# Performance work log

Hardware: AMD Instinct MI355X
Metric: run time of the kernel (lower is better)

## Reference

```python
import jax, jax.numpy as jnp
import numpy as np

N = 50000      # nodes
E = 800000     # directed edges (before self-loops)
IN = 128       # input feature dim
HID = 32       # per-head hidden channels
HEADS = 4
OUT = 16       # output classes
NEG_SLOPE = 0.2


def setup_inputs() -> dict:
    key = jax.random.key(0)
    ks = jax.random.split(key, 14)
    x = jax.random.normal(ks[0], (N, IN), jnp.float32)
    edge_index = jax.random.randint(ks[1], (2, E), 0, N, dtype=jnp.int64)

    def glorot(k, shape):
        fan = shape[0] + shape[-1]
        s = np.sqrt(6.0 / fan).astype(np.float32)
        return jax.random.uniform(k, shape, jnp.float32, -s, s)

    return {
        "x": x,
        "edge_index": edge_index,
        # layer 0: IN -> HEADS*HID
        "W1": glorot(ks[2], (IN, HEADS * HID)),
        "a_src1": glorot(ks[3], (HEADS, HID)),
        "a_dst1": glorot(ks[4], (HEADS, HID)),
        "b1": jnp.zeros((HEADS * HID,), jnp.float32),
        # layer 1: HEADS*HID -> HEADS*HID
        "W2": glorot(ks[5], (HEADS * HID, HEADS * HID)),
        "a_src2": glorot(ks[6], (HEADS, HID)),
        "a_dst2": glorot(ks[7], (HEADS, HID)),
        "b2": jnp.zeros((HEADS * HID,), jnp.float32),
        # layer 2: HEADS*HID -> OUT, heads=1
        "W3": glorot(ks[8], (HEADS * HID, OUT)),
        "a_src3": glorot(ks[9], (1, OUT)),
        "a_dst3": glorot(ks[10], (1, OUT)),
        "b3": jnp.zeros((OUT,), jnp.float32),
    }


def _gat_layer(x, src, dst, W, a_s, a_d, b):
    """One PyG-style GATConv (eval mode). src/dst include self-loops."""
    H, C = a_s.shape
    h = (x @ W).reshape(N, H, C)                       # [N,H,C]
    e_src = jnp.einsum('nhc,hc->nh', h, a_s)           # [N,H]
    e_dst = jnp.einsum('nhc,hc->nh', h, a_d)
    e = jax.nn.leaky_relu(e_src[src] + e_dst[dst], NEG_SLOPE)   # [E',H]
    # segment softmax over incoming edges of each target node
    m = jax.ops.segment_max(e, dst, num_segments=N)    # [N,H]
    p = jnp.exp(e - m[dst])
    denom = jax.ops.segment_sum(p, dst, num_segments=N)
    alpha = p / (denom[dst] + 1e-16)                   # [E',H]
    out = jax.ops.segment_sum(alpha[:, :, None] * h[src], dst, num_segments=N)
    return out.reshape(N, H * C) + b


def reference(x, edge_index, W1, a_src1, a_dst1, b1, W2, a_src2, a_dst2, b2,
              W3, a_src3, a_dst3, b3):
    loops = jnp.arange(N, dtype=edge_index.dtype)
    src = jnp.concatenate([edge_index[0], loops])
    dst = jnp.concatenate([edge_index[1], loops])
    h = jax.nn.relu(_gat_layer(x, src, dst, W1, a_src1, a_dst1, b1))
    h = jax.nn.relu(_gat_layer(h, src, dst, W2, a_src2, a_dst2, b2))
    return _gat_layer(h, src, dst, W3, a_src3, a_dst3, b3)   # [N, OUT]
```

## Files before the change

### kernel.cpp

```cpp
#include <hip/hip_runtime.h>

#define NODES 50000
#define EDGES 800000
#define EPLUS (EDGES + NODES)
#define GEMMBLK 782
#define FILLBLK 3328
#define CHUNKE 2048
#define NRANGE 8
#define RSPAN 6250
#define CAP 64

typedef __attribute__((ext_vector_type(8))) short bf16x8;
typedef __attribute__((ext_vector_type(4))) float f32x4;
typedef __attribute__((ext_vector_type(4))) short short4v;

__device__ __forceinline__ float ld_f(const void* p, int isbf, size_t i) {
    if (isbf) return __uint_as_float(((unsigned)((const unsigned short*)p)[i]) << 16);
    return ((const float*)p)[i];
}
__device__ __forceinline__ int ld_idx(const int* ei, int i64, int elem) {
    int v = i64 ? ei[(size_t)elem * 2] : ei[elem];
    v = v < 0 ? 0 : v;
    return v >= NODES ? NODES - 1 : v;
}
__device__ __forceinline__ unsigned short f2bf(float f) {
    unsigned u = __float_as_uint(f);
    u = u + 0x7FFFu + ((u >> 16) & 1u);
    return (unsigned short)(u >> 16);
}
__device__ __forceinline__ unsigned pack2bf(float a, float b) {
    return (unsigned)f2bf(a) | ((unsigned)f2bf(b) << 16);
}
__device__ __forceinline__ float bflo(unsigned u) { return __uint_as_float(u << 16); }
__device__ __forceinline__ float bfhi(unsigned u) { return __uint_as_float(u & 0xFFFF0000u); }

__device__ __forceinline__ void detect_flags(const unsigned* xw, const int* eiw,
                                             int* sh, int& isbf, int& i64) {
    const int t = threadIdx.x;
    if (t < 2) sh[t] = 0;
    __syncthreads();
    if (t < 256) {
        unsigned lo = xw[t] & 0xFFFFu;
        int e = (int)((lo >> 7) & 0xFF);
        if (lo == 0u || (e >= 90 && e <= 140)) atomicAdd(&sh[0], 1);
    }
    if (t < 64) {
        if (eiw[2 * t + 1] == 0) atomicAdd(&sh[1], 1);
    }
    __syncthreads();
    isbf = sh[0] > 200 ? 1 : 0;
    i64  = sh[1] > 48 ? 1 : 0;
}

#define O_W1 0
#define O_AS1 16384
#define O_AD1 16512
#define O_B1 16640
#define O_W2 16768
#define O_AS2 33152
#define O_AD2 33280
#define O_B2 33408
#define O_W3 33536
#define O_AS3 35584
#define O_AD3 35600
#define O_B3 35616
#define W_TOTAL 35632

#define PB_CNT 196
#define PB_WC 140
#define PB_F1 64
#define PB_F2 64
#define PB_F3 8
#define PREP_GRID (PB_CNT + PB_WC + PB_F1 + PB_F2 + PB_F3)

__global__ __launch_bounds__(256) void k_prep(
        const unsigned* __restrict__ xraw, const int* __restrict__ ei,
        const void* w1, const void* as1, const void* ad1, const void* b1,
        const void* w2, const void* as2, const void* ad2, const void* b2,
        const void* w3, const void* as3, const void* ad3, const void* b3,
        float* __restrict__ Wc, int* __restrict__ cnt,
        unsigned short* __restrict__ W1fh, unsigned short* __restrict__ W1fl,
        unsigned short* __restrict__ W2fh, unsigned short* __restrict__ W2fl,
        unsigned short* __restrict__ W3fh, unsigned short* __restrict__ W3fl) {
    __shared__ int sh[2];
    const int t = threadIdx.x;
    int isbf, i64;
    detect_flags(xraw, ei, sh, isbf, i64);
    (void)i64;

    int b = blockIdx.x;
    if (b < PB_CNT) {
        int i = b * 256 + t;
        if (i < NODES) cnt[i] = 0;
        return;
    }
    b -= PB_CNT;
    if (b < PB_WC) {
        const int f = b * 256 + t;
        if (f < W_TOTAL) {
            const int sz[12] = {16384,128,128,128,16384,128,128,128,2048,16,16,16};
            const void* ps[12] = {w1,as1,ad1,b1,w2,as2,ad2,b2,w3,as3,ad3,b3};
            int off = 0;
#pragma unroll
            for (int s = 0; s < 12; ++s) {
                if (f >= off && f < off + sz[s]) Wc[f] = ld_f(ps[s], isbf, f - off);
                off += sz[s];
            }
        }
        return;
    }
    b -= PB_WC;
    const void* wsrc; unsigned short *fh, *fl; int ncols; int e;
    if (b < PB_F1)                { wsrc = w1; fh = W1fh; fl = W1fl; ncols = 128; e = b * 256 + t; }
    else if (b < PB_F1 + PB_F2)   { wsrc = w2; fh = W2fh; fl = W2fl; ncols = 128; e = (b - PB_F1) * 256 + t; }
    else                          { wsrc = w3; fh = W3fh; fl = W3fl; ncols = 16;  e = (b - PB_F1 - PB_F2) * 256 + t; }
    const int j = e & 7, l = (e >> 3) & 63;
    int nf, kc;
    if (ncols == 128) { nf = (e >> 9) & 7; kc = e >> 12; }
    else              { nf = 0;            kc = (e >> 9) & 3; }
    const int k = kc * 32 + (l >> 4) * 4 + (j & 3) + (j >> 2) * 16;
    const int n = nf * 16 + (l & 15);
    const float v = ld_f(wsrc, isbf, (size_t)k * ncols + n);
    const unsigned short hi = f2bf(v);
    const float res = v - __uint_as_float(((unsigned)hi) << 16);
    fh[e] = hi;
    fl[e] = f2bf(res);
}

__global__ __launch_bounds__(256, 4) void k_fillgemm1(
        const unsigned* __restrict__ xraw, const int* __restrict__ ei,
        const unsigned short* __restrict__ W1fh, const unsigned short* __restrict__ W1fl,
        const float* __restrict__ Wc,
        unsigned short* __restrict__ hout, float* __restrict__ es, float* __restrict__ ed,
        int* __restrict__ cnt, unsigned short* __restrict__ col) {
    __shared__ int sh[2];
    const int t = threadIdx.x;
    int isbf, i64;
    detect_flags(xraw, ei, sh, isbf, i64);

    if (blockIdx.x >= GEMMBLK) {
        const int fb = blockIdx.x - GEMMBLK;
        const int r  = blockIdx.x & 7;
        const int chunk = fb >> 3;
        const int lo = r * RSPAN, hi = lo + RSPAN;
        const int base = chunk * CHUNKE;
#pragma unroll
        for (int it = 0; it < CHUNKE / 256; ++it) {
            const int e = base + it * 256 + t;
            if (e >= EPLUS) continue;
            int s, d;
            if (e < EDGES) {
                d = ld_idx(ei, i64, EDGES + e);
                if (d < lo || d >= hi) continue;
                s = ld_idx(ei, i64, e);
            } else {
                s = d = e - EDGES;
                if (d < lo || d >= hi) continue;
            }
            int slot = atomicAdd(&cnt[d], 1);
            if (slot < CAP) col[d * CAP + slot] = (unsigned short)s;
        }
        return;
    }

    __shared__ unsigned short Ah[4 * 64 * 8];
    __shared__ unsigned short Al[4 * 64 * 8];
    const int rowBase = blockIdx.x * 64;
    const int w = t >> 6, lane = t & 63;

    f32x4 acc[4][2];
#pragma unroll
    for (int mf = 0; mf < 4; ++mf)
#pragma unroll
        for (int nn = 0; nn < 2; ++nn) acc[mf][nn] = (f32x4){0.f, 0.f, 0.f, 0.f};

    for (int kc = 0; kc < 4; ++kc) {
        __syncthreads();
#pragma unroll
        for (int u = 0; u < 2; ++u) {
            const int f = t + 256 * u;
            const int r = f >> 3, c4 = f & 7;
            int gr = rowBase + r; if (gr >= NODES) gr = NODES - 1;
            const int mf = r >> 4;
            const int l  = (r & 15) + 16 * (c4 & 3);
            const int j0 = 4 * (c4 >> 2);
            const int di = (mf * 64 + l) * 8 + j0;
            if (!isbf) {
                f32x4 v = __builtin_nontemporal_load(
                    (const f32x4*)((const float*)xraw + (size_t)gr * 128 + kc * 32 + c4 * 4));
                const unsigned short h0 = f2bf(v[0]), h1 = f2bf(v[1]), h2 = f2bf(v[2]), h3 = f2bf(v[3]);
                short4v hv = {(short)h0, (short)h1, (short)h2, (short)h3};
                *(short4v*)&Ah[di] = hv;
                short4v lv = {(short)f2bf(v[0] - __uint_as_float((unsigned)h0 << 16)),
                              (short)f2bf(v[1] - __uint_as_float((unsigned)h1 << 16)),
                              (short)f2bf(v[2] - __uint_as_float((unsigned)h2 << 16)),
                              (short)f2bf(v[3] - __uint_as_float((unsigned)h3 << 16))};
                *(short4v*)&Al[di] = lv;
            } else {
                short4v v = __builtin_nontemporal_load(
                    (const short4v*)((const unsigned short*)xraw + (size_t)gr * 128 + kc * 32 + c4 * 4));
                *(short4v*)&Ah[di] = v;
            }
        }
        __syncthreads();
        const int nA = 2 * w, nB = 2 * w + 1;
        const bf16x8 bh0 = *(const bf16x8*)(W1fh + (((size_t)kc * 8 + nA) * 64 + lane) * 8);
        const bf16x8 bh1 = *(const bf16x8*)(W1fh + (((size_t)kc * 8 + nB) * 64 + lane) * 8);
        const bf16x8 bl0 = *(const bf16x8*)(W1fl + (((size_t)kc * 8 + nA) * 64 + lane) * 8);
        const bf16x8 bl1 = *(const bf16x8*)(W1fl + (((size_t)kc * 8 + nB) * 64 + lane) * 8);
#pragma unroll
        for (int mf = 0; mf < 4; ++mf) {
            const bf16x8 ah = *(const bf16x8*)&Ah[(mf * 64 + lane) * 8];
            acc[mf][0] = __builtin_amdgcn_mfma_f32_16x16x32_bf16(ah, bh0, acc[mf][0], 0, 0, 0);
            acc[mf][1] = __builtin_amdgcn_mfma_f32_16x16x32_bf16(ah, bh1, acc[mf][1], 0, 0, 0);
            if (!isbf) {
                const bf16x8 al = *(const bf16x8*)&Al[(mf * 64 + lane) * 8];
                acc[mf][0] = __builtin_amdgcn_mfma_f32_16x16x32_bf16(ah, bl0, acc[mf][0], 0, 0, 0);
                acc[mf][1] = __builtin_amdgcn_mfma_f32_16x16x32_bf16(ah, bl1, acc[mf][1], 0, 0, 0);
                acc[mf][0] = __builtin_amdgcn_mfma_f32_16x16x32_bf16(al, bh0, acc[mf][0], 0, 0, 0);
                acc[mf][1] = __builtin_amdgcn_mfma_f32_16x16x32_bf16(al, bh1, acc[mf][1], 0, 0, 0);
            }
        }
    }

    const int colA = 32 * w + (lane & 15), colB = colA + 16;
    const float asA = Wc[O_AS1 + colA], asB = Wc[O_AS1 + colB];
    const float adA = Wc[O_AD1 + colA], adB = Wc[O_AD1 + colB];
    const int g = lane >> 4;
#pragma unroll
    for (int mf = 0; mf < 4; ++mf) {
#pragma unroll
        for (int r = 0; r < 4; ++r) {
            const int row = rowBase + mf * 16 + 4 * g + r;
            const bool ok = row < NODES;
            const float vA = acc[mf][0][r], vB = acc[mf][1][r];
            if (ok) {
                hout[(size_t)row * 128 + colA] = f2bf(vA);
                hout[(size_t)row * 128 + colB] = f2bf(vB);
            }
            float se = vA * asA + vB * asB;
            float sd = vA * adA + vB * adB;
#pragma unroll
            for (int off = 1; off < 16; off <<= 1) {
                se += __shfl_xor(se, off);
                sd += __shfl_xor(sd, off);
            }
            if (ok && (lane & 15) == 0) {
                es[row * 4 + w] = se;
                ed[row * 4 + w] = sd;
            }
        }
    }
}

__device__ __forceinline__ void gather4_node(
        int nd, const int* __restrict__ cnt, const unsigned short* __restrict__ col,
        const float* __restrict__ esi, const float* __restrict__ edi,
        const uint4* __restrict__ h4, int esub, int c, int myh,
        float a[8], float& den) {
    int deg = cnt[nd]; deg = deg < CAP ? deg : CAP;
    const int start = nd * CAP;
    const float edh = edi[nd * 4 + myh];
#pragma unroll
    for (int j = 0; j < 8; ++j) a[j] = 0.f;
    den = 0.f;
    int e = esub;
    for (; e + 12 < deg; e += 16) {
        int s0 = col[start + e];
        int s1 = col[start + e + 4];
        int s2 = col[start + e + 8];
        int s3 = col[start + e + 12];
        uint4 u0 = h4[(size_t)s0 * 16 + c];
        uint4 u1 = h4[(size_t)s1 * 16 + c];
        uint4 u2 = h4[(size_t)s2 * 16 + c];
        uint4 u3 = h4[(size_t)s3 * 16 + c];
        float v0 = esi[s0 * 4 + myh] + edh; v0 = v0 > 0.f ? v0 : 0.2f * v0;
        float v1 = esi[s1 * 4 + myh] + edh; v1 = v1 > 0.f ? v1 : 0.2f * v1;
        float v2 = esi[s2 * 4 + myh] + edh; v2 = v2 > 0.f ? v2 : 0.2f * v2;
        float v3 = esi[s3 * 4 + myh] + edh; v3 = v3 > 0.f ? v3 : 0.2f * v3;
        float p0 = __expf(v0), p1 = __expf(v1), p2 = __expf(v2), p3 = __expf(v3);
        den += (p0 + p1) + (p2 + p3);
        a[0] += p0 * bflo(u0.x) + p1 * bflo(u1.x) + p2 * bflo(u2.x) + p3 * bflo(u3.x);
        a[1] += p0 * bfhi(u0.x) + p1 * bfhi(u1.x) + p2 * bfhi(u2.x) + p3 * bfhi(u3.x);
        a[2] += p0 * bflo(u0.y) + p1 * bflo(u1.y) + p2 * bflo(u2.y) + p3 * bflo(u3.y);
        a[3] += p0 * bfhi(u0.y) + p1 * bfhi(u1.y) + p2 * bfhi(u2.y) + p3 * bfhi(u3.y);
        a[4] += p0 * bflo(u0.z) + p1 * bflo(u1.z) + p2 * bflo(u2.z) + p3 * bflo(u3.z);
        a[5] += p0 * bfhi(u0.z) + p1 * bfhi(u1.z) + p2 * bfhi(u2.z) + p3 * bfhi(u3.z);
        a[6] += p0 * bflo(u0.w) + p1 * bflo(u1.w) + p2 * bflo(u2.w) + p3 * bflo(u3.w);
        a[7] += p0 * bfhi(u0.w) + p1 * bfhi(u1.w) + p2 * bfhi(u2.w) + p3 * bfhi(u3.w);
    }
    for (; e + 4 < deg; e += 8) {
        int s0 = col[start + e];
        int s1 = col[start + e + 4];
        uint4 u0 = h4[(size_t)s0 * 16 + c];
        uint4 u1 = h4[(size_t)s1 * 16 + c];
        float v0 = esi[s0 * 4 + myh] + edh; v0 = v0 > 0.f ? v0 : 0.2f * v0;
        float v1 = esi[s1 * 4 + myh] + edh; v1 = v1 > 0.f ? v1 : 0.2f * v1;
        float p0 = __expf(v0);
        float p1 = __expf(v1);
        den += p0 + p1;
        a[0] += p0 * bflo(u0.x) + p1 * bflo(u1.x);
        a[1] += p0 * bfhi(u0.x) + p1 * bfhi(u1.x);
        a[2] += p0 * bflo(u0.y) + p1 * bflo(u1.y);
        a[3] += p0 * bfhi(u0.y) + p1 * bfhi(u1.y);
        a[4] += p0 * bflo(u0.z) + p1 * bflo(u1.z);
        a[5] += p0 * bfhi(u0.z) + p1 * bfhi(u1.z);
        a[6] += p0 * bflo(u0.w) + p1 * bflo(u1.w);
        a[7] += p0 * bfhi(u0.w) + p1 * bfhi(u1.w);
    }
    for (; e < deg; e += 4) {
        int s0 = col[start + e];
        uint4 u0 = h4[(size_t)s0 * 16 + c];
        float v0 = esi[s0 * 4 + myh] + edh; v0 = v0 > 0.f ? v0 : 0.2f * v0;
        float p0 = __expf(v0);
        den += p0;
        a[0] += p0 * bflo(u0.x);
        a[1] += p0 * bfhi(u0.x);
        a[2] += p0 * bflo(u0.y);
        a[3] += p0 * bfhi(u0.y);
        a[4] += p0 * bflo(u0.z);
        a[5] += p0 * bfhi(u0.z);
        a[6] += p0 * bflo(u0.w);
        a[7] += p0 * bfhi(u0.w);
    }
    den += __shfl_xor(den, 16);
    den += __shfl_xor(den, 32);
#pragma unroll
    for (int j = 0; j < 8; ++j) {
        a[j] += __shfl_xor(a[j], 16);
        a[j] += __shfl_xor(a[j], 32);
    }
}

__global__ __launch_bounds__(512, 4) void k_gg128(
        const int* __restrict__ cnt, const unsigned short* __restrict__ col,
        const float* __restrict__ esi, const float* __restrict__ edi,
        const unsigned short* __restrict__ hfeat, const float* __restrict__ bias,
        const unsigned short* __restrict__ Wfh, const unsigned short* __restrict__ Wfl,
        const float* __restrict__ a_s, const float* __restrict__ a_d,
        unsigned short* __restrict__ hout, float* __restrict__ eso, float* __restrict__ edo) {
    __shared__ unsigned short X2f[4 * 4 * 64 * 8];
    const int t = threadIdx.x;
    const int v = t >> 6, lane = t & 63;
    const int rowBase = blockIdx.x * 64;

    const int esub = lane >> 4;
    const int c = lane & 15;
    const int myh = c >> 2;
    const uint4* __restrict__ h4 = (const uint4*)hfeat;
    for (int i = 0; i < 8; ++i) {
        const int r = v * 8 + i;
        const int nd = rowBase + r;
        if (nd >= NODES) break;
        float a[8], den;
        gather4_node(nd, cnt, col, esi, edi, h4, esub, c, myh, a, den);
        if (esub == 0) {
            const float inv = 1.f / (den + 1e-16f);
            float4 b0 = ((const float4*)bias)[c * 2];
            float4 b1 = ((const float4*)bias)[c * 2 + 1];
            float o0 = a[0]*inv + b0.x, o1 = a[1]*inv + b0.y;
            float o2 = a[2]*inv + b0.z, o3 = a[3]*inv + b0.w;
            float o4 = a[4]*inv + b1.x, o5 = a[5]*inv + b1.y;
            float o6 = a[6]*inv + b1.z, o7 = a[7]*inv + b1.w;
            o0 = o0 > 0.f ? o0 : 0.f;  o1 = o1 > 0.f ? o1 : 0.f;
            o2 = o2 > 0.f ? o2 : 0.f;  o3 = o3 > 0.f ? o3 : 0.f;
            o4 = o4 > 0.f ? o4 : 0.f;  o5 = o5 > 0.f ? o5 : 0.f;
            o6 = o6 > 0.f ? o6 : 0.f;  o7 = o7 > 0.f ? o7 : 0.f;
            const int cc = c & 3;
            const int kc = c >> 2;
            const int mf = r >> 4;
            const int l0 = (r & 15) + 16 * ((2 * cc) & 3);
            const int l1 = (r & 15) + 16 * ((2 * cc + 1) & 3);
            const int j0 = (cc < 2) ? 0 : 4;
            short4v w0 = {(short)f2bf(o0), (short)f2bf(o1), (short)f2bf(o2), (short)f2bf(o3)};
            short4v w1 = {(short)f2bf(o4), (short)f2bf(o5), (short)f2bf(o6), (short)f2bf(o7)};
            *(short4v*)&X2f[((kc * 4 + mf) * 64 + l0) * 8 + j0] = w0;
            *(short4v*)&X2f[((kc * 4 + mf) * 64 + l1) * 8 + j0] = w1;
        }
    }
    __syncthreads();

    const int vr = v >> 2, vc = v & 3;
    f32x4 acc[2][2];
#pragma unroll
    for (int m = 0; m < 2; ++m)
#pragma unroll
        for (int nn = 0; nn < 2; ++nn) acc[m][nn] = (f32x4){0.f, 0.f, 0.f, 0.f};

    const int nA = 2 * vc, nB = 2 * vc + 1;
#pragma unroll
    for (int kc = 0; kc < 4; ++kc) {
        const bf16x8 bh0 = *(const bf16x8*)(Wfh + (((size_t)kc * 8 + nA) * 64 + lane) * 8);
        const bf16x8 bh1 = *(const bf16x8*)(Wfh + (((size_t)kc * 8 + nB) * 64 + lane) * 8);
        const bf16x8 bl0 = *(const bf16x8*)(Wfl + (((size_t)kc * 8 + nA) * 64 + lane) * 8);
        const bf16x8 bl1 = *(const bf16x8*)(Wfl + (((size_t)kc * 8 + nB) * 64 + lane) * 8);
#pragma unroll
        for (int m = 0; m < 2; ++m) {
            const int mf = 2 * vr + m;
            const bf16x8 ah = *(const bf16x8*)&X2f[((kc * 4 + mf) * 64 + lane) * 8];
            acc[m][0] = __builtin_amdgcn_mfma_f32_16x16x32_bf16(ah, bh0, acc[m][0], 0, 0, 0);
            acc[m][1] = __builtin_amdgcn_mfma_f32_16x16x32_bf16(ah, bh1, acc[m][1], 0, 0, 0);
            acc[m][0] = __builtin_amdgcn_mfma_f32_16x16x32_bf16(ah, bl0, acc[m][0], 0, 0, 0);
            acc[m][1] = __builtin_amdgcn_mfma_f32_16x16x32_bf16(ah, bl1, acc[m][1], 0, 0, 0);
        }
    }

    const int colA = 32 * vc + (lane & 15), colB = colA + 16;
    const float asA = a_s[colA], asB = a_s[colB];
    const float adA = a_d[colA], adB = a_d[colB];
    const int g = lane >> 4;
#pragma unroll
    for (int m = 0; m < 2; ++m) {
#pragma unroll
        for (int r = 0; r < 4; ++r) {
            const int row = rowBase + (2 * vr + m) * 16 + 4 * g + r;
            const bool ok = row < NODES;
            const float vA = acc[m][0][r], vB = acc[m][1][r];
            if (ok) {
                hout[(size_t)row * 128 + colA] = f2bf(vA);
                hout[(size_t)row * 128 + colB] = f2bf(vB);
            }
            float se = vA * asA + vB * asB;
            float sd = vA * adA + vB * adB;
#pragma unroll
            for (int off = 1; off < 16; off <<= 1) {
                se += __shfl_xor(se, off);
                sd += __shfl_xor(sd, off);
            }
            if (ok && (lane & 15) == 0) {
                eso[row * 4 + vc] = se;
                edo[row * 4 + vc] = sd;
            }
        }
    }
}

__global__ __launch_bounds__(512, 4) void k_gg16(
        const int* __restrict__ cnt, const unsigned short* __restrict__ col,
        const float* __restrict__ esi, const float* __restrict__ edi,
        const unsigned short* __restrict__ hfeat, const float* __restrict__ bias,
        const unsigned short* __restrict__ Wfh, const unsigned short* __restrict__ Wfl,
        const float* __restrict__ a_s, const float* __restrict__ a_d,
        unsigned short* __restrict__ hout, float* __restrict__ eso, float* __restrict__ edo) {
    __shared__ unsigned short X2f[4 * 4 * 64 * 8];
    const int t = threadIdx.x;
    const int v = t >> 6, lane = t & 63;
    const int rowBase = blockIdx.x * 64;

    const int esub = lane >> 4;
    const int c = lane & 15;
    const int myh = c >> 2;
    const uint4* __restrict__ h4 = (const uint4*)hfeat;
    for (int i = 0; i < 8; ++i) {
        const int r = v * 8 + i;
        const int nd = rowBase + r;
        if (nd >= NODES) break;
        float a[8], den;
        gather4_node(nd, cnt, col, esi, edi, h4, esub, c, myh, a, den);
        if (esub == 0) {
            const float inv = 1.f / (den + 1e-16f);
            float4 b0 = ((const float4*)bias)[c * 2];
            float4 b1 = ((const float4*)bias)[c * 2 + 1];
            float o0 = a[0]*inv + b0.x, o1 = a[1]*inv + b0.y;
            float o2 = a[2]*inv + b0.z, o3 = a[3]*inv + b0.w;
            float o4 = a[4]*inv + b1.x, o5 = a[5]*inv + b1.y;
            float o6 = a[6]*inv + b1.z, o7 = a[7]*inv + b1.w;
            o0 = o0 > 0.f ? o0 : 0.f;  o1 = o1 > 0.f ? o1 : 0.f;
            o2 = o2 > 0.f ? o2 : 0.f;  o3 = o3 > 0.f ? o3 : 0.f;
            o4 = o4 > 0.f ? o4 : 0.f;  o5 = o5 > 0.f ? o5 : 0.f;
            o6 = o6 > 0.f ? o6 : 0.f;  o7 = o7 > 0.f ? o7 : 0.f;
            const int cc = c & 3;
            const int kc = c >> 2;
            const int mf = r >> 4;
            const int l0 = (r & 15) + 16 * ((2 * cc) & 3);
            const int l1 = (r & 15) + 16 * ((2 * cc + 1) & 3);
            const int j0 = (cc < 2) ? 0 : 4;
            short4v w0 = {(short)f2bf(o0), (short)f2bf(o1), (short)f2bf(o2), (short)f2bf(o3)};
            short4v w1 = {(short)f2bf(o4), (short)f2bf(o5), (short)f2bf(o6), (short)f2bf(o7)};
            *(short4v*)&X2f[((kc * 4 + mf) * 64 + l0) * 8 + j0] = w0;
            *(short4v*)&X2f[((kc * 4 + mf) * 64 + l1) * 8 + j0] = w1;
        }
    }
    __syncthreads();

    if (v < 4) {
        f32x4 acc = (f32x4){0.f, 0.f, 0.f, 0.f};
#pragma unroll
        for (int kc = 0; kc < 4; ++kc) {
            const bf16x8 bh = *(const bf16x8*)(Wfh + ((size_t)kc * 64 + lane) * 8);
            const bf16x8 bl = *(const bf16x8*)(Wfl + ((size_t)kc * 64 + lane) * 8);
            const bf16x8 ah = *(const bf16x8*)&X2f[((kc * 4 + v) * 64 + lane) * 8];
            acc = __builtin_amdgcn_mfma_f32_16x16x32_bf16(ah, bh, acc, 0, 0, 0);
            acc = __builtin_amdgcn_mfma_f32_16x16x32_bf16(ah, bl, acc, 0, 0, 0);
        }
        const int cc = lane & 15, g = lane >> 4;
        const float asv = a_s[cc], adv = a_d[cc];
#pragma unroll
        for (int r = 0; r < 4; ++r) {
            const int row = rowBase + v * 16 + 4 * g + r;
            const bool ok = row < NODES;
            if (ok) hout[(size_t)row * 16 + cc] = f2bf(acc[r]);
            float se = acc[r] * asv;
            float sd = acc[r] * adv;
#pragma unroll
            for (int off = 1; off < 16; off <<= 1) {
                se += __shfl_xor(se, off);
                sd += __shfl_xor(sd, off);
            }
            if (ok && cc == 0) { eso[row] = se; edo[row] = sd; }
        }
    }
}

__global__ void k_gather1(const int* __restrict__ cnt, const unsigned short* __restrict__ col,
                          const float* __restrict__ es, const float* __restrict__ ed,
                          const unsigned short* __restrict__ hfeat,
                          const float* __restrict__ bias, float* __restrict__ outf) {
    const int nd = blockIdx.x * 4 + (threadIdx.x >> 6);
    if (nd >= NODES) return;
    const int lane = threadIdx.x & 63;
    int deg = cnt[nd]; deg = deg < CAP ? deg : CAP;
    const int start = nd * CAP;

    const float edv = ed[nd];
    const int esub = lane >> 3;
    const int c = lane & 7;
    const unsigned* __restrict__ h1 = (const unsigned*)hfeat;
    float a0 = 0.f, a1 = 0.f, den = 0.f;

    int e = esub;
    for (; e + 24 < deg; e += 32) {
        int s0 = col[start + e];
        int s1 = col[start + e + 8];
        int s2 = col[start + e + 16];
        int s3 = col[start + e + 24];
        unsigned u0 = h1[(size_t)s0 * 8 + c];
        unsigned u1 = h1[(size_t)s1 * 8 + c];
        unsigned u2 = h1[(size_t)s2 * 8 + c];
        unsigned u3 = h1[(size_t)s3 * 8 + c];
        float v0 = es[s0] + edv; v0 = v0 > 0.f ? v0 : 0.2f * v0;
        float v1 = es[s1] + edv; v1 = v1 > 0.f ? v1 : 0.2f * v1;
        float v2 = es[s2] + edv; v2 = v2 > 0.f ? v2 : 0.2f * v2;
        float v3 = es[s3] + edv; v3 = v3 > 0.f ? v3 : 0.2f * v3;
        float p0 = __expf(v0), p1 = __expf(v1), p2 = __expf(v2), p3 = __expf(v3);
        den += (p0 + p1) + (p2 + p3);
        a0 += p0 * bflo(u0) + p1 * bflo(u1) + p2 * bflo(u2) + p3 * bflo(u3);
        a1 += p0 * bfhi(u0) + p1 * bfhi(u1) + p2 * bfhi(u2) + p3 * bfhi(u3);
    }
    for (; e + 8 < deg; e += 16) {
        int s0 = col[start + e];
        int s1 = col[start + e + 8];
        unsigned u0 = h1[(size_t)s0 * 8 + c];
        unsigned u1 = h1[(size_t)s1 * 8 + c];
        float v0 = es[s0] + edv; v0 = v0 > 0.f ? v0 : 0.2f * v0;
        float v1 = es[s1] + edv; v1 = v1 > 0.f ? v1 : 0.2f * v1;
        float p0 = __expf(v0);
        float p1 = __expf(v1);
        den += p0 + p1;
        a0 += p0 * bflo(u0) + p1 * bflo(u1);
        a1 += p0 * bfhi(u0) + p1 * bfhi(u1);
    }
    for (; e < deg; e += 8) {
        int s0 = col[start + e];
        unsigned u0 = h1[(size_t)s0 * 8 + c];
        float v0 = es[s0] + edv; v0 = v0 > 0.f ? v0 : 0.2f * v0;
        float p0 = __expf(v0);
        den += p0;
        a0 += p0 * bflo(u0);
        a1 += p0 * bfhi(u0);
    }
    den += __shfl_xor(den, 8);  a0 += __shfl_xor(a0, 8);  a1 += __shfl_xor(a1, 8);
    den += __shfl_xor(den, 16); a0 += __shfl_xor(a0, 16); a1 += __shfl_xor(a1, 16);
    den += __shfl_xor(den, 32); a0 += __shfl_xor(a0, 32); a1 += __shfl_xor(a1, 32);
    if (lane < 8) {
        const float inv = 1.f / (den + 1e-16f);
        float2 b = ((const float2*)bias)[c];
        ((float2*)outf)[(size_t)nd * 8 + c] = make_float2(a0 * inv + b.x, a1 * inv + b.y);
    }
}

extern "C" void kernel_launch(void* const* d_in, const int* in_sizes, int n_in,
                              void* d_out, int out_size, void* d_ws, size_t ws_size,
                              hipStream_t stream) {
    const int* ei = (const int*)d_in[1];
    const unsigned* xraw = (const unsigned*)d_in[0];
    float* out = (float*)d_out;

    char* p = (char*)d_ws;
    unsigned short* h2  = (unsigned short*)p; p += (size_t)NODES * 128 * 2;
    unsigned short* h1  = (unsigned short*)p; p += (size_t)NODES * 128 * 2;
    float*          es1 = (float*)p;          p += (size_t)NODES * 4 * 4;
    float*          ed1 = (float*)p;          p += (size_t)NODES * 4 * 4;
    float*          Wc  = (float*)p;          p += (size_t)W_TOTAL * 4;
    int*            cnt = (int*)p;            p += (size_t)NODES * 4;
    unsigned short* col = (unsigned short*)p; p += (size_t)NODES * CAP * 2;
    unsigned short* W1fh = (unsigned short*)p; p += 16384 * 2;
    unsigned short* W1fl = (unsigned short*)p; p += 16384 * 2;
    unsigned short* W2fh = (unsigned short*)p; p += 16384 * 2;
    unsigned short* W2fl = (unsigned short*)p; p += 16384 * 2;
    unsigned short* W3fh = (unsigned short*)p; p += 2048 * 2;
    unsigned short* W3fl = (unsigned short*)p; p += 2048 * 2;
    float*          es2 = (float*)p;          p += (size_t)NODES * 4 * 4;
    float*          ed2 = (float*)p;          p += (size_t)NODES * 4 * 4;

    k_prep<<<PREP_GRID, 256, 0, stream>>>(
        xraw, ei,
        d_in[2], d_in[3], d_in[4], d_in[5],
        d_in[6], d_in[7], d_in[8], d_in[9],
        d_in[10], d_in[11], d_in[12], d_in[13],
        Wc, cnt, W1fh, W1fl, W2fh, W2fl, W3fh, W3fl);

    k_fillgemm1<<<GEMMBLK + FILLBLK, 256, 0, stream>>>(
        xraw, ei, W1fh, W1fl, Wc, h1, es1, ed1, cnt, col);

    k_gg128<<<GEMMBLK, 512, 0, stream>>>(cnt, col, es1, ed1, h1, Wc + O_B1,
                                         W2fh, W2fl, Wc + O_AS2, Wc + O_AD2,
                                         h2, es2, ed2);
    k_gg16<<<GEMMBLK, 512, 0, stream>>>(cnt, col, es2, ed2, h2, Wc + O_B2,
                                        W3fh, W3fl, Wc + O_AS3, Wc + O_AD3,
                                        h1, es1, ed1);
    const int ggrid = (NODES + 3) / 4;
    k_gather1<<<ggrid, 256, 0, stream>>>(cnt, col, es1, ed1, h1, Wc + O_B3, out);
}
```

Baseline: 283.6 us.

## Halve gather-GEMM block size to 32 rows and drop 4-way unrolled gather loops

The fused gather+GEMM kernels for layers 2 and 3 now use 256-thread blocks covering 32 nodes instead of 512 threads covering 64. The grid doubles, and the MFMA work is remapped so each of the 4 waves handles two column fragments across both row fragments. The 4-way unrolled edge loops in the gather helpers are removed, which lowers register pressure and code size, leaving 2-way unrolled and scalar tails. The aim is better occupancy and load balance for an irregular, latency-bound gather. The cost is less memory-level parallelism per thread, and the weight fragments are reloaded by twice as many blocks.

```diff
diff --git a/kernel.cpp b/kernel.cpp
--- a/kernel.cpp
+++ b/kernel.cpp
@@ -4,6 +4,7 @@
 #define EDGES 800000
 #define EPLUS (EDGES + NODES)
 #define GEMMBLK 782
+#define GGBLK 1563
 #define FILLBLK 3328
 #define CHUNKE 2048
 #define NRANGE 8
@@ -27,9 +28,6 @@
     unsigned u = __float_as_uint(f);
     u = u + 0x7FFFu + ((u >> 16) & 1u);
     return (unsigned short)(u >> 16);
-}
-__device__ __forceinline__ unsigned pack2bf(float a, float b) {
-    return (unsigned)f2bf(a) | ((unsigned)f2bf(b) << 16);
 }
 __device__ __forceinline__ float bflo(unsigned u) { return __uint_as_float(u << 16); }
 __device__ __forceinline__ float bfhi(unsigned u) { return __uint_as_float(u & 0xFFFF0000u); }
@@ -265,30 +263,6 @@
     for (int j = 0; j < 8; ++j) a[j] = 0.f;
     den = 0.f;
     int e = esub;
-    for (; e + 12 < deg; e += 16) {
-        int s0 = col[start + e];
-        int s1 = col[start + e + 4];
-        int s2 = col[start + e + 8];
-        int s3 = col[start + e + 12];
-        uint4 u0 = h4[(size_t)s0 * 16 + c];
-        uint4 u1 = h4[(size_t)s1 * 16 + c];
-        uint4 u2 = h4[(size_t)s2 * 16 + c];
-        uint4 u3 = h4[(size_t)s3 * 16 + c];
-        float v0 = esi[s0 * 4 + myh] + edh; v0 = v0 > 0.f ? v0 : 0.2f * v0;
-        float v1 = esi[s1 * 4 + myh] + edh; v1 = v1 > 0.f ? v1 : 0.2f * v1;
-        float v2 = esi[s2 * 4 + myh] + edh; v2 = v2 > 0.f ? v2 : 0.2f * v2;
-        float v3 = esi[s3 * 4 + myh] + edh; v3 = v3 > 0.f ? v3 : 0.2f * v3;
-        float p0 = __expf(v0), p1 = __expf(v1), p2 = __expf(v2), p3 = __expf(v3);
-        den += (p0 + p1) + (p2 + p3);
-        a[0] += p0 * bflo(u0.x) + p1 * bflo(u1.x) + p2 * bflo(u2.x) + p3 * bflo(u3.x);
-        a[1] += p0 * bfhi(u0.x) + p1 * bfhi(u1.x) + p2 * bfhi(u2.x) + p3 * bfhi(u3.x);
-        a[2] += p0 * bflo(u0.y) + p1 * bflo(u1.y) + p2 * bflo(u2.y) + p3 * bflo(u3.y);
-        a[3] += p0 * bfhi(u0.y) + p1 * bfhi(u1.y) + p2 * bfhi(u2.y) + p3 * bfhi(u3.y);
-        a[4] += p0 * bflo(u0.z) + p1 * bflo(u1.z) + p2 * bflo(u2.z) + p3 * bflo(u3.z);
-        a[5] += p0 * bfhi(u0.z) + p1 * bfhi(u1.z) + p2 * bfhi(u2.z) + p3 * bfhi(u3.z);
-        a[6] += p0 * bflo(u0.w) + p1 * bflo(u1.w) + p2 * bflo(u2.w) + p3 * bflo(u3.w);
-        a[7] += p0 * bfhi(u0.w) + p1 * bfhi(u1.w) + p2 * bfhi(u2.w) + p3 * bfhi(u3.w);
-    }
     for (; e + 4 < deg; e += 8) {
         int s0 = col[start + e];
         int s1 = col[start + e + 4];
@@ -332,17 +306,44 @@
     }
 }
 
-__global__ __launch_bounds__(512, 4) void k_gg128(
+#define NMF 2
+__device__ __forceinline__ void place_frag(
+        unsigned short* __restrict__ X2f, int r, int c,
+        const float a[8], float den, const float* __restrict__ bias) {
+    const float inv = 1.f / (den + 1e-16f);
+    float4 b0 = ((const float4*)bias)[c * 2];
+    float4 b1 = ((const float4*)bias)[c * 2 + 1];
+    float o0 = a[0]*inv + b0.x, o1 = a[1]*inv + b0.y;
+    float o2 = a[2]*inv + b0.z, o3 = a[3]*inv + b0.w;
+    float o4 = a[4]*inv + b1.x, o5 = a[5]*inv + b1.y;
+    float o6 = a[6]*inv + b1.z, o7 = a[7]*inv + b1.w;
+    o0 = o0 > 0.f ? o0 : 0.f;  o1 = o1 > 0.f ? o1 : 0.f;
+    o2 = o2 > 0.f ? o2 : 0.f;  o3 = o3 > 0.f ? o3 : 0.f;
+    o4 = o4 > 0.f ? o4 : 0.f;  o5 = o5 > 0.f ? o5 : 0.f;
+    o6 = o6 > 0.f ? o6 : 0.f;  o7 = o7 > 0.f ? o7 : 0.f;
+    const int cc = c & 3;
+    const int kc = c >> 2;
+    const int mf = r >> 4;
+    const int l0 = (r & 15) + 16 * ((2 * cc) & 3);
+    const int l1 = (r & 15) + 16 * ((2 * cc + 1) & 3);
+    const int j0 = (cc < 2) ? 0 : 4;
+    short4v w0 = {(short)f2bf(o0), (short)f2bf(o1), (short)f2bf(o2), (short)f2bf(o3)};
+    short4v w1 = {(short)f2bf(o4), (short)f2bf(o5), (short)f2bf(o6), (short)f2bf(o7)};
+    *(short4v*)&X2f[((kc * NMF + mf) * 64 + l0) * 8 + j0] = w0;
+    *(short4v*)&X2f[((kc * NMF + mf) * 64 + l1) * 8 + j0] = w1;
+}
+
+__global__ __launch_bounds__(256, 8) void k_gg128(
         const int* __restrict__ cnt, const unsigned short* __restrict__ col,
         const float* __restrict__ esi, const float* __restrict__ edi,
         const unsigned short* __restrict__ hfeat, const float* __restrict__ bias,
         const unsigned short* __restrict__ Wfh, const unsigned short* __restrict__ Wfl,
         const float* __restrict__ a_s, const float* __restrict__ a_d,
         unsigned short* __restrict__ hout, float* __restrict__ eso, float* __restrict__ edo) {
-    __shared__ unsigned short X2f[4 * 4 * 64 * 8];
+    __shared__ unsigned short X2f[4 * NMF * 64 * 8];
     const int t = threadIdx.x;
     const int v = t >> 6, lane = t & 63;
-    const int rowBase = blockIdx.x * 64;
+    const int rowBase = blockIdx.x * 32;
 
     const int esub = lane >> 4;
     const int c = lane & 15;
@@ -354,40 +355,17 @@
         if (nd >= NODES) break;
         float a[8], den;
         gather4_node(nd, cnt, col, esi, edi, h4, esub, c, myh, a, den);
-        if (esub == 0) {
-            const float inv = 1.f / (den + 1e-16f);
-            float4 b0 = ((const float4*)bias)[c * 2];
-            float4 b1 = ((const float4*)bias)[c * 2 + 1];
-            float o0 = a[0]*inv + b0.x, o1 = a[1]*inv + b0.y;
-            float o2 = a[2]*inv + b0.z, o3 = a[3]*inv + b0.w;
-            float o4 = a[4]*inv + b1.x, o5 = a[5]*inv + b1.y;
-            float o6 = a[6]*inv + b1.z, o7 = a[7]*inv + b1.w;
-            o0 = o0 > 0.f ? o0 : 0.f;  o1 = o1 > 0.f ? o1 : 0.f;
-            o2 = o2 > 0.f ? o2 : 0.f;  o3 = o3 > 0.f ? o3 : 0.f;
-            o4 = o4 > 0.f ? o4 : 0.f;  o5 = o5 > 0.f ? o5 : 0.f;
-            o6 = o6 > 0.f ? o6 : 0.f;  o7 = o7 > 0.f ? o7 : 0.f;
-            const int cc = c & 3;
-            const int kc = c >> 2;
-            const int mf = r >> 4;
-            const int l0 = (r & 15) + 16 * ((2 * cc) & 3);
-            const int l1 = (r & 15) + 16 * ((2 * cc + 1) & 3);
-            const int j0 = (cc < 2) ? 0 : 4;
-            short4v w0 = {(short)f2bf(o0), (short)f2bf(o1), (short)f2bf(o2), (short)f2bf(o3)};
-            short4v w1 = {(short)f2bf(o4), (short)f2bf(o5), (short)f2bf(o6), (short)f2bf(o7)};
-            *(short4v*)&X2f[((kc * 4 + mf) * 64 + l0) * 8 + j0] = w0;
-            *(short4v*)&X2f[((kc * 4 + mf) * 64 + l1) * 8 + j0] = w1;
-        }
+        if (esub == 0) place_frag(X2f, r, c, a, den, bias);
     }
     __syncthreads();
 
-    const int vr = v >> 2, vc = v & 3;
     f32x4 acc[2][2];
 #pragma unroll
     for (int m = 0; m < 2; ++m)
 #pragma unroll
         for (int nn = 0; nn < 2; ++nn) acc[m][nn] = (f32x4){0.f, 0.f, 0.f, 0.f};
 
-    const int nA = 2 * vc, nB = 2 * vc + 1;
+    const int nA = 2 * v, nB = 2 * v + 1;
 #pragma unroll
     for (int kc = 0; kc < 4; ++kc) {
         const bf16x8 bh0 = *(const bf16x8*)(Wfh + (((size_t)kc * 8 + nA) * 64 + lane) * 8);
@@ -396,8 +374,7 @@
         const bf16x8 bl1 = *(const bf16x8*)(Wfl + (((size_t)kc * 8 + nB) * 64 + lane) * 8);
 #pragma unroll
         for (int m = 0; m < 2; ++m) {
-            const int mf = 2 * vr + m;
-            const bf16x8 ah = *(const bf16x8*)&X2f[((kc * 4 + mf) * 64 + lane) * 8];
+            const bf16x8 ah = *(const bf16x8*)&X2f[((kc * NMF + m) * 64 + lane) * 8];
             acc[m][0] = __builtin_amdgcn_mfma_f32_16x16x32_bf16(ah, bh0, acc[m][0], 0, 0, 0);
             acc[m][1] = __builtin_amdgcn_mfma_f32_16x16x32_bf16(ah, bh1, acc[m][1], 0, 0, 0);
             acc[m][0] = __builtin_amdgcn_mfma_f32_16x16x32_bf16(ah, bl0, acc[m][0], 0, 0, 0);
@@ -405,7 +382,7 @@
         }
     }
 
-    const int colA = 32 * vc + (lane & 15), colB = colA + 16;
+    const int colA = 32 * v + (lane & 15), colB = colA + 16;
     const float asA = a_s[colA], asB = a_s[colB];
     const float adA = a_d[colA], adB = a_d[colB];
     const int g = lane >> 4;
@@ -413,7 +390,7 @@
     for (int m = 0; m < 2; ++m) {
 #pragma unroll
         for (int r = 0; r < 4; ++r) {
-            const int row = rowBase + (2 * vr + m) * 16 + 4 * g + r;
+            const int row = rowBase + m * 16 + 4 * g + r;
             const bool ok = row < NODES;
             const float vA = acc[m][0][r], vB = acc[m][1][r];
             if (ok) {
@@ -428,24 +405,24 @@
                 sd += __shfl_xor(sd, off);
             }
             if (ok && (lane & 15) == 0) {
-                eso[row * 4 + vc] = se;
-                edo[row * 4 + vc] = sd;
-            }
-        }
-    }
-}
-
-__global__ __launch_bounds__(512, 4) void k_gg16(
+                eso[row * 4 + v] = se;
+                edo[row * 4 + v] = sd;
+            }
+        }
+    }
+}
+
+__global__ __launch_bounds__(256, 8) void k_gg16(
         const int* __restrict__ cnt, const unsigned short* __restrict__ col,
         const float* __restrict__ esi, const float* __restrict__ edi,
         const unsigned short* __restrict__ hfeat, const float* __restrict__ bias,
         const unsigned short* __restrict__ Wfh, const unsigned short* __restrict__ Wfl,
         const float* __restrict__ a_s, const float* __restrict__ a_d,
         unsigned short* __restrict__ hout, float* __restrict__ eso, float* __restrict__ edo) {
-    __shared__ unsigned short X2f[4 * 4 * 64 * 8];
+    __shared__ unsigned short X2f[4 * NMF * 64 * 8];
     const int t = threadIdx.x;
     const int v = t >> 6, lane = t & 63;
-    const int rowBase = blockIdx.x * 64;
+    const int rowBase = blockIdx.x * 32;
 
     const int esub = lane >> 4;
     const int c = lane & 15;
@@ -457,39 +434,17 @@
         if (nd >= NODES) break;
         float a[8], den;
         gather4_node(nd, cnt, col, esi, edi, h4, esub, c, myh, a, den);
-        if (esub == 0) {
-            const float inv = 1.f / (den + 1e-16f);
-            float4 b0 = ((const float4*)bias)[c * 2];
-            float4 b1 = ((const float4*)bias)[c * 2 + 1];
-            float o0 = a[0]*inv + b0.x, o1 = a[1]*inv + b0.y;
-            float o2 = a[2]*inv + b0.z, o3 = a[3]*inv + b0.w;
-            float o4 = a[4]*inv + b1.x, o5 = a[5]*inv + b1.y;
-            float o6 = a[6]*inv + b1.z, o7 = a[7]*inv + b1.w;
-            o0 = o0 > 0.f ? o0 : 0.f;  o1 = o1 > 0.f ? o1 : 0.f;
-            o2 = o2 > 0.f ? o2 : 0.f;  o3 = o3 > 0.f ? o3 : 0.f;
-            o4 = o4 > 0.f ? o4 : 0.f;  o5 = o5 > 0.f ? o5 : 0.f;
-            o6 = o6 > 0.f ? o6 : 0.f;  o7 = o7 > 0.f ? o7 : 0.f;
-            const int cc = c & 3;
-            const int kc = c >> 2;
-            const int mf = r >> 4;
-            const int l0 = (r & 15) + 16 * ((2 * cc) & 3);
-            const int l1 = (r & 15) + 16 * ((2 * cc + 1) & 3);
-            const int j0 = (cc < 2) ? 0 : 4;
-            short4v w0 = {(short)f2bf(o0), (short)f2bf(o1), (short)f2bf(o2), (short)f2bf(o3)};
-            short4v w1 = {(short)f2bf(o4), (short)f2bf(o5), (short)f2bf(o6), (short)f2bf(o7)};
-            *(short4v*)&X2f[((kc * 4 + mf) * 64 + l0) * 8 + j0] = w0;
-            *(short4v*)&X2f[((kc * 4 + mf) * 64 + l1) * 8 + j0] = w1;
-        }
+        if (esub == 0) place_frag(X2f, r, c, a, den, bias);
     }
     __syncthreads();
 
-    if (v < 4) {
+    if (v < 2) {
         f32x4 acc = (f32x4){0.f, 0.f, 0.f, 0.f};
 #pragma unroll
         for (int kc = 0; kc < 4; ++kc) {
             const bf16x8 bh = *(const bf16x8*)(Wfh + ((size_t)kc * 64 + lane) * 8);
             const bf16x8 bl = *(const bf16x8*)(Wfl + ((size_t)kc * 64 + lane) * 8);
-            const bf16x8 ah = *(const bf16x8*)&X2f[((kc * 4 + v) * 64 + lane) * 8];
+            const bf16x8 ah = *(const bf16x8*)&X2f[((kc * NMF + v) * 64 + lane) * 8];
             acc = __builtin_amdgcn_mfma_f32_16x16x32_bf16(ah, bh, acc, 0, 0, 0);
             acc = __builtin_amdgcn_mfma_f32_16x16x32_bf16(ah, bl, acc, 0, 0, 0);
         }
@@ -529,24 +484,6 @@
     float a0 = 0.f, a1 = 0.f, den = 0.f;
 
     int e = esub;
-    for (; e + 24 < deg; e += 32) {
-        int s0 = col[start + e];
-        int s1 = col[start + e + 8];
-        int s2 = col[start + e + 16];
-        int s3 = col[start + e + 24];
-        unsigned u0 = h1[(size_t)s0 * 8 + c];
-        unsigned u1 = h1[(size_t)s1 * 8 + c];
-        unsigned u2 = h1[(size_t)s2 * 8 + c];
-        unsigned u3 = h1[(size_t)s3 * 8 + c];
-        float v0 = es[s0] + edv; v0 = v0 > 0.f ? v0 : 0.2f * v0;
-        float v1 = es[s1] + edv; v1 = v1 > 0.f ? v1 : 0.2f * v1;
-        float v2 = es[s2] + edv; v2 = v2 > 0.f ? v2 : 0.2f * v2;
-        float v3 = es[s3] + edv; v3 = v3 > 0.f ? v3 : 0.2f * v3;
-        float p0 = __expf(v0), p1 = __expf(v1), p2 = __expf(v2), p3 = __expf(v3);
-        den += (p0 + p1) + (p2 + p3);
-        a0 += p0 * bflo(u0) + p1 * bflo(u1) + p2 * bflo(u2) + p3 * bflo(u3);
-        a1 += p0 * bfhi(u0) + p1 * bfhi(u1) + p2 * bfhi(u2) + p3 * bfhi(u3);
-    }
     for (; e + 8 < deg; e += 16) {
         int s0 = col[start + e];
         int s1 = col[start + e + 8];
@@ -613,12 +550,12 @@
     k_fillgemm1<<<GEMMBLK + FILLBLK, 256, 0, stream>>>(
         xraw, ei, W1fh, W1fl, Wc, h1, es1, ed1, cnt, col);
 
-    k_gg128<<<GEMMBLK, 512, 0, stream>>>(cnt, col, es1, ed1, h1, Wc + O_B1,
-                                         W2fh, W2fl, Wc + O_AS2, Wc + O_AD2,
-                                         h2, es2, ed2);
-    k_gg16<<<GEMMBLK, 512, 0, stream>>>(cnt, col, es2, ed2, h2, Wc + O_B2,
-                                        W3fh, W3fl, Wc + O_AS3, Wc + O_AD3,
-                                        h1, es1, ed1);
+    k_gg128<<<GGBLK, 256, 0, stream>>>(cnt, col, es1, ed1, h1, Wc + O_B1,
+                                       W2fh, W2fl, Wc + O_AS2, Wc + O_AD2,
+                                       h2, es2, ed2);
+    k_gg16<<<GGBLK, 256, 0, stream>>>(cnt, col, es2, ed2, h2, Wc + O_B2,
+                                      W3fh, W3fl, Wc + O_AS3, Wc + O_AD3,
+                                      h1, es1, ed1);
     const int ggrid = (NODES + 3) / 4;
     k_gather1<<<ggrid, 256, 0, stream>>>(cnt, col, es1, ed1, h1, Wc + O_B3, out);
 }
```

Result: faster. 244.4 us (-13.8%).
